# Kernel tuning notes

Hardware: AMD Instinct MI355X
Metric: run time of the kernel (lower is better)

## Reference

```python
import jax, jax.numpy as jnp
import numpy as np

N, E = 50000, 800000
D, H, EDIM, DFF = 128, 8, 16, 512
C = D // H  # per-head channels
NEG_SLOPE_GAT = 0.2
NEG_SLOPE = 0.01
EPS_LN = 1e-6


def layer_norm(x, g, b):
    mu = x.mean(-1, keepdims=True)
    sd = x.std(-1, keepdims=True, ddof=1)  # torch std default (unbiased)
    return g * (x - mu) / (sd + EPS_LN) + b


def gat_conv(x, ei, ew, W, a_src, a_dst, We, a_e, bias):
    # PyG GATConv with edge_dim, concat=True, eval mode (no dropout)
    n = x.shape[0]
    xh = (x @ W).reshape(n, H, C)            # [N,H,C]
    s_src = (xh * a_src).sum(-1)             # [N,H]
    s_dst = (xh * a_dst).sum(-1)             # [N,H]
    eh = (ew @ We).reshape(-1, H, C)         # [E,H,C]
    s_e = (eh * a_e).sum(-1)                 # [E,H]
    src, dst = ei[0], ei[1]
    alpha = jax.nn.leaky_relu(s_src[src] + s_dst[dst] + s_e, NEG_SLOPE_GAT)  # [E,H]
    # segment softmax over destination nodes
    m = jax.ops.segment_max(alpha, dst, num_segments=n)
    alpha = jnp.exp(alpha - m[dst])
    z = jax.ops.segment_sum(alpha, dst, num_segments=n)
    alpha = alpha / (z[dst] + 1e-16)
    msg = xh[src] * alpha[..., None]         # [E,H,C]
    out = jax.ops.segment_sum(msg, dst, num_segments=n)  # [N,H,C]
    return out.reshape(n, H * C) + bias


def setup_inputs() -> dict:
    key = jax.random.key(0)
    ks = jax.random.split(key, 32)
    p = lambda k, sh: (jax.random.normal(k, sh, dtype=jnp.float32) * 0.02)
    inp = {
        "nf": jax.random.normal(ks[0], (N, D), dtype=jnp.float32),
        "ei": jax.random.randint(ks[1], (2, E), 0, N, dtype=jnp.int32),
        "ew": jax.random.normal(ks[2], (E, EDIM), dtype=jnp.float32),
        # GATConv 1
        "W1": p(ks[3], (D, H * C)), "as1": p(ks[4], (H, C)), "ad1": p(ks[5], (H, C)),
        "We1": p(ks[6], (EDIM, H * C)), "ae1": p(ks[7], (H, C)), "b1": jnp.zeros((H * C,), jnp.float32),
        "g1": jnp.ones((D,), jnp.float32), "be1": jnp.zeros((D,), jnp.float32),
        # GATConv 2
        "W2": p(ks[8], (D, H * C)), "as2": p(ks[9], (H, C)), "ad2": p(ks[10], (H, C)),
        "We2": p(ks[11], (EDIM, H * C)), "ae2": p(ks[12], (H, C)), "b2": jnp.zeros((H * C,), jnp.float32),
        "g2": jnp.ones((D,), jnp.float32), "be2": jnp.zeros((D,), jnp.float32),
        # FFN + norm3
        "Wf1": p(ks[13], (D, DFF)), "bf1": jnp.zeros((DFF,), jnp.float32),
        "Wf2": p(ks[14], (DFF, D)), "bf2": jnp.zeros((D,), jnp.float32),
        "g3": jnp.ones((D,), jnp.float32), "be3": jnp.zeros((D,), jnp.float32),
    }
    return inp


def reference(nf, ei, ew, W1, as1, ad1, We1, ae1, b1, g1, be1,
              W2, as2, ad2, We2, ae2, b2, g2, be2,
              Wf1, bf1, Wf2, bf2, g3, be3):
    # gnn_mode == 'res', eval mode (dropout = identity)
    h = gat_conv(nf, ei, ew, W1, as1, ad1, We1, ae1, b1)
    nf = nf + jax.nn.leaky_relu(layer_norm(h, g1, be1), NEG_SLOPE)
    h = gat_conv(nf, ei, ew, W2, as2, ad2, We2, ae2, b2)
    nf = nf + jax.nn.leaky_relu(layer_norm(h, g2, be2), NEG_SLOPE)
    ff = jax.nn.relu(nf @ Wf1 + bf1) @ Wf2 + bf2
    nf = nf + jax.nn.leaky_relu(layer_norm(ff, g3, be3), NEG_SLOPE)
    return nf
```

## Files before the change

### kernel.cpp

```cpp
#include <hip/hip_runtime.h>
#include <hip/hip_bf16.h>

#define NN 50000
#define NE 800000
#define DD 128
#define HH 8
#define CC 16
#define DFF 512
#define ED 16
#define SCAN_NB ((NN + 255) / 256)

typedef __attribute__((ext_vector_type(8))) short bf16x8;
typedef __attribute__((ext_vector_type(4))) float f32x4;

union U8 { bf16x8 v; unsigned short s[8]; };

__device__ inline unsigned short f2bf(float f) {
    union { float f; unsigned u; } v; v.f = f;
    return (unsigned short)((v.u + 0x7fffu + ((v.u >> 16) & 1u)) >> 16);
}
__device__ inline float bf2f(unsigned s) {
    union { unsigned u; float f; } v; v.u = s << 16;
    return v.f;
}

__global__ void zero_int_k(int* __restrict__ a, int n) {
    int i = blockIdx.x * 256 + threadIdx.x;
    if (i < n) a[i] = 0;
}

__global__ void cvtpack_k(const float* __restrict__ W, unsigned short* __restrict__ Wpk,
                          int K, int N) {
    int idx = blockIdx.x * 256 + threadIdx.x;
    if (idx >= K * N) return;
    int e = idx & 7;
    int l = (idx >> 3) & 63;
    int r = idx >> 9;
    int n16 = N >> 4;
    int jc = r % n16;
    int kt = r / n16;
    int k = kt * 32 + (l >> 4) * 8 + e;
    int n = jc * 16 + (l & 15);
    Wpk[idx] = f2bf(W[(size_t)k * N + n]);
}

__global__ void count_k(const int* __restrict__ dst, int* __restrict__ cnt) {
    int e = blockIdx.x * 256 + threadIdx.x;
    if (e < NE) atomicAdd(&cnt[dst[e]], 1);
}

__global__ void blksum_k(const int* __restrict__ cnt, int* __restrict__ partials) {
    int i = blockIdx.x * 256 + threadIdx.x;
    int v = (i < NN) ? cnt[i] : 0;
#pragma unroll
    for (int m = 1; m < 64; m <<= 1) v += __shfl_xor(v, m, 64);
    __shared__ int ws[4];
    if ((threadIdx.x & 63) == 0) ws[threadIdx.x >> 6] = v;
    __syncthreads();
    if (threadIdx.x == 0) partials[blockIdx.x] = ws[0] + ws[1] + ws[2] + ws[3];
}

__global__ void scanpart_k(int* __restrict__ partials) {
    __shared__ int buf[256];
    int t = threadIdx.x;
    int v = (t < SCAN_NB) ? partials[t] : 0;
    buf[t] = v;
    __syncthreads();
    for (int off = 1; off < 256; off <<= 1) {
        int u = (t >= off) ? buf[t - off] : 0;
        __syncthreads();
        buf[t] += u;
        __syncthreads();
    }
    if (t < SCAN_NB) partials[t] = buf[t] - v;
}

__global__ void scanapply_k(const int* __restrict__ cnt, const int* __restrict__ partials,
                            int* __restrict__ row_start, int* __restrict__ cursor) {
    __shared__ int buf[256];
    int t = threadIdx.x;
    int i = blockIdx.x * 256 + t;
    int v = (i < NN) ? cnt[i] : 0;
    buf[t] = v;
    __syncthreads();
    for (int off = 1; off < 256; off <<= 1) {
        int u = (t >= off) ? buf[t - off] : 0;
        __syncthreads();
        buf[t] += u;
        __syncthreads();
    }
    int excl = buf[t] - v + partials[blockIdx.x];
    if (i < NN) {
        row_start[i] = excl;
        cursor[i] = excl;
        if (i == NN - 1) row_start[NN] = excl + v;
    }
}

__global__ void scatter_k(const int* __restrict__ ei, int* __restrict__ cursor,
                          int2* __restrict__ es_eid) {
    int e = blockIdx.x * 256 + threadIdx.x;
    if (e >= NE) return;
    int s = ei[e];
    int d = ei[NE + e];
    int pos = atomicAdd(&cursor[d], 1);
    es_eid[pos] = make_int2(s, e);
}

__global__ void se2_k(const float* __restrict__ ew, const int2* __restrict__ es_eid,
                      const float* __restrict__ We1, const float* __restrict__ ae1,
                      const float* __restrict__ We2, const float* __restrict__ ae2,
                      float* __restrict__ s_e1, float* __restrict__ s_e2) {
    __shared__ float A1[ED * HH], A2[ED * HH];
    int t = threadIdx.x;
    if (t < 128) {
        int k = t >> 3, h = t & 7;
        float s = 0.f;
#pragma unroll
        for (int c = 0; c < CC; c++) s += We1[k * DD + h * CC + c] * ae1[h * CC + c];
        A1[t] = s;
    } else {
        int u = t - 128;
        int k = u >> 3, h = u & 7;
        float s = 0.f;
#pragma unroll
        for (int c = 0; c < CC; c++) s += We2[k * DD + h * CC + c] * ae2[h * CC + c];
        A2[u] = s;
    }
    __syncthreads();
    int p = blockIdx.x * 256 + t;
    if (p >= NE) return;
    int eid = es_eid[p].y;
    const float* ep = &ew[(size_t)eid * ED];
    float4 v0 = *(const float4*)(ep);
    float4 v1 = *(const float4*)(ep + 4);
    float4 v2 = *(const float4*)(ep + 8);
    float4 v3 = *(const float4*)(ep + 12);
    float ev[16] = {v0.x, v0.y, v0.z, v0.w, v1.x, v1.y, v1.z, v1.w,
                    v2.x, v2.y, v2.z, v2.w, v3.x, v3.y, v3.z, v3.w};
    float o1[8] = {0, 0, 0, 0, 0, 0, 0, 0};
    float o2[8] = {0, 0, 0, 0, 0, 0, 0, 0};
#pragma unroll
    for (int k = 0; k < 16; k++) {
        float v = ev[k];
#pragma unroll
        for (int h = 0; h < 8; h++) {
            o1[h] += v * A1[k * 8 + h];
            o2[h] += v * A2[k * 8 + h];
        }
    }
    *(float4*)&s_e1[(size_t)p * 8]     = make_float4(o1[0], o1[1], o1[2], o1[3]);
    *(float4*)&s_e1[(size_t)p * 8 + 4] = make_float4(o1[4], o1[5], o1[6], o1[7]);
    *(float4*)&s_e2[(size_t)p * 8]     = make_float4(o2[0], o2[1], o2[2], o2[3]);
    *(float4*)&s_e2[(size_t)p * 8 + 4] = make_float4(o2[4], o2[5], o2[6], o2[7]);
}

__global__ __launch_bounds__(256) void gemm_mfma_k(const float* __restrict__ X,
                                                   const unsigned short* __restrict__ Wpk,
                                                   unsigned short* __restrict__ Ybf) {
    __shared__ char Xl[128 * 256];
    int t = threadIdx.x;
    int nb0 = blockIdx.x * 128;
    for (int c = t; c < 2048; c += 256) {
        int row = c >> 4, cb = c & 15;
        int n = nb0 + row;
        U8 u;
        if (n < NN) {
            const float* xp = &X[(size_t)n * DD + cb * 8];
            float4 a = *(const float4*)xp;
            float4 b = *(const float4*)(xp + 4);
            u.s[0] = f2bf(a.x); u.s[1] = f2bf(a.y); u.s[2] = f2bf(a.z); u.s[3] = f2bf(a.w);
            u.s[4] = f2bf(b.x); u.s[5] = f2bf(b.y); u.s[6] = f2bf(b.z); u.s[7] = f2bf(b.w);
        } else {
#pragma unroll
            for (int q = 0; q < 8; q++) u.s[q] = 0;
        }
        int byte = (row * 256 + cb * 16) ^ ((row & 7) << 4);
        *(bf16x8*)&Xl[byte] = u.v;
    }
    __syncthreads();
    int w = t >> 6, l = t & 63;
    int lrow = l & 15, lq = l >> 4;
    int r0 = (w & 1) * 64, c0 = (w >> 1) * 64;
    f32x4 acc[4][4];
#pragma unroll
    for (int i = 0; i < 4; i++)
#pragma unroll
        for (int j = 0; j < 4; j++) acc[i][j] = (f32x4){0.f, 0.f, 0.f, 0.f};
#pragma unroll
    for (int ks = 0; ks < 4; ks++) {
        int k0 = ks * 32;
        bf16x8 af[4], bq[4];
#pragma unroll
        for (int i = 0; i < 4; i++) {
            int rr = r0 + i * 16 + lrow;
            int byte = (rr * 256 + k0 * 2 + lq * 16) ^ ((rr & 7) << 4);
            af[i] = *(const bf16x8*)&Xl[byte];
        }
#pragma unroll
        for (int j = 0; j < 4; j++) {
            int j16 = (c0 >> 4) + j;
            bq[j] = *(const bf16x8*)&Wpk[(((size_t)ks * 8 + j16) * 64 + l) * 8];
        }
#pragma unroll
        for (int i = 0; i < 4; i++)
#pragma unroll
            for (int j = 0; j < 4; j++)
                acc[i][j] = __builtin_amdgcn_mfma_f32_16x16x32_bf16(af[i], bq[j], acc[i][j], 0, 0, 0);
    }
#pragma unroll
    for (int i = 0; i < 4; i++) {
#pragma unroll
        for (int j = 0; j < 4; j++) {
#pragma unroll
            for (int q = 0; q < 4; q++) {
                int n = nb0 + r0 + i * 16 + lq * 4 + q;
                if (n < NN) Ybf[(size_t)n * DD + c0 + j * 16 + lrow] = f2bf(acc[i][j][q]);
            }
        }
    }
}

__global__ void ssd_k(const unsigned short* __restrict__ xh_bf, const float* __restrict__ a_src,
                      const float* __restrict__ a_dst, float* __restrict__ s_src,
                      float* __restrict__ s_dst) {
    __shared__ float as[128], ad[128];
    if (threadIdx.x < 128) {
        as[threadIdx.x] = a_src[threadIdx.x];
        ad[threadIdx.x] = a_dst[threadIdx.x];
    }
    __syncthreads();
    int idx = blockIdx.x * 256 + threadIdx.x;
    if (idx >= NN * HH) return;
    int n = idx >> 3, h = idx & 7;
    const unsigned short* x = &xh_bf[(size_t)n * DD + h * CC];
    U8 u0, u1;
    u0.v = *(const bf16x8*)(x);
    u1.v = *(const bf16x8*)(x + 8);
    float s1 = 0.f, s2 = 0.f;
#pragma unroll
    for (int c = 0; c < 8; c++) {
        float v = bf2f(u0.s[c]);
        s1 += v * as[h * CC + c];
        s2 += v * ad[h * CC + c];
    }
#pragma unroll
    for (int c = 0; c < 8; c++) {
        float v = bf2f(u1.s[c]);
        s1 += v * as[h * CC + 8 + c];
        s2 += v * ad[h * CC + 8 + c];
    }
    s_src[idx] = s1;
    s_dst[idx] = s2;
}

__global__ __launch_bounds__(256) void agg_ln_k(const int* __restrict__ row_start,
                                                const int2* __restrict__ es_eid,
                                                const float* __restrict__ s_src,
                                                const float* __restrict__ s_dst,
                                                const float* __restrict__ s_e,
                                                const unsigned short* __restrict__ xh_bf,
                                                const float* __restrict__ bias,
                                                const float* __restrict__ g,
                                                const float* __restrict__ be,
                                                const float* __restrict__ res,
                                                float* __restrict__ outNf) {
    int wid = (blockIdx.x * 256 + threadIdx.x) >> 6;
    if (wid >= NN) return;
    int lane = threadIdx.x & 63;
    int h = lane >> 3;
    float sdst = s_dst[wid * 8 + h];
    int beg = row_start[wid], end = row_start[wid + 1];
    float acc0 = 0.f, acc1 = 0.f, z = 0.f;
    int p = beg;
    for (; p + 4 <= end; p += 4) {
        int q0 = es_eid[p].x;
        int q1 = es_eid[p + 1].x;
        int q2 = es_eid[p + 2].x;
        int q3 = es_eid[p + 3].x;
        float a0 = s_src[q0 * 8 + h] + sdst + s_e[(size_t)p * 8 + h];
        float a1 = s_src[q1 * 8 + h] + sdst + s_e[(size_t)(p + 1) * 8 + h];
        float a2 = s_src[q2 * 8 + h] + sdst + s_e[(size_t)(p + 2) * 8 + h];
        float a3 = s_src[q3 * 8 + h] + sdst + s_e[(size_t)(p + 3) * 8 + h];
        unsigned u0 = *(const unsigned*)&xh_bf[(size_t)q0 * DD + lane * 2];
        unsigned u1 = *(const unsigned*)&xh_bf[(size_t)q1 * DD + lane * 2];
        unsigned u2 = *(const unsigned*)&xh_bf[(size_t)q2 * DD + lane * 2];
        unsigned u3 = *(const unsigned*)&xh_bf[(size_t)q3 * DD + lane * 2];
        a0 = (a0 > 0.f) ? a0 : 0.2f * a0;
        a1 = (a1 > 0.f) ? a1 : 0.2f * a1;
        a2 = (a2 > 0.f) ? a2 : 0.2f * a2;
        a3 = (a3 > 0.f) ? a3 : 0.2f * a3;
        float e0 = __expf(a0);
        float e1 = __expf(a1);
        float e2 = __expf(a2);
        float e3 = __expf(a3);
        z += (e0 + e1) + (e2 + e3);
        acc0 = fmaf(e0, bf2f(u0 & 0xffffu), acc0);
        acc1 = fmaf(e0, bf2f(u0 >> 16), acc1);
        acc0 = fmaf(e1, bf2f(u1 & 0xffffu), acc0);
        acc1 = fmaf(e1, bf2f(u1 >> 16), acc1);
        acc0 = fmaf(e2, bf2f(u2 & 0xffffu), acc0);
        acc1 = fmaf(e2, bf2f(u2 >> 16), acc1);
        acc0 = fmaf(e3, bf2f(u3 & 0xffffu), acc0);
        acc1 = fmaf(e3, bf2f(u3 >> 16), acc1);
    }
    for (; p < end; p++) {
        int q0 = es_eid[p].x;
        float a0 = s_src[q0 * 8 + h] + sdst + s_e[(size_t)p * 8 + h];
        unsigned u0 = *(const unsigned*)&xh_bf[(size_t)q0 * DD + lane * 2];
        a0 = (a0 > 0.f) ? a0 : 0.2f * a0;
        float e0 = __expf(a0);
        z += e0;
        acc0 = fmaf(e0, bf2f(u0 & 0xffffu), acc0);
        acc1 = fmaf(e0, bf2f(u0 >> 16), acc1);
    }
    float inv = 1.f / (z + 1e-16f);
    float2 b = *(const float2*)&bias[lane * 2];
    float x0 = acc0 * inv + b.x;
    float x1 = acc1 * inv + b.y;
    float s = x0 + x1;
    float q = x0 * x0 + x1 * x1;
#pragma unroll
    for (int m = 1; m < 64; m <<= 1) {
        s += __shfl_xor(s, m, 64);
        q += __shfl_xor(q, m, 64);
    }
    float mu = s * (1.f / 128.f);
    float var = (q - 128.f * mu * mu) * (1.f / 127.f);
    float sd = sqrtf(fmaxf(var, 0.f));
    float invs = 1.f / (sd + 1e-6f);
    float2 gg = *(const float2*)&g[lane * 2];
    float2 bb = *(const float2*)&be[lane * 2];
    float y0 = gg.x * (x0 - mu) * invs + bb.x;
    float y1 = gg.y * (x1 - mu) * invs + bb.y;
    y0 = (y0 > 0.f) ? y0 : 0.01f * y0;
    y1 = (y1 > 0.f) ? y1 : 0.01f * y1;
    float2 r = *(const float2*)&res[(size_t)wid * DD + lane * 2];
    *(float2*)&outNf[(size_t)wid * DD + lane * 2] = make_float2(r.x + y0, r.y + y1);
}

__global__ __launch_bounds__(256) void ln_k(const float* __restrict__ hin,
                                            const float* __restrict__ bias,
                                            const float* __restrict__ g,
                                            const float* __restrict__ be,
                                            const float* __restrict__ res,
                                            float* __restrict__ out) {
    int wid = (blockIdx.x * 256 + threadIdx.x) >> 6;
    if (wid >= NN) return;
    int lane = threadIdx.x & 63;
    float2 x = *(const float2*)&hin[(size_t)wid * DD + lane * 2];
    float2 b = *(const float2*)&bias[lane * 2];
    x.x += b.x;
    x.y += b.y;
    float s = x.x + x.y;
    float q = x.x * x.x + x.y * x.y;
#pragma unroll
    for (int m = 1; m < 64; m <<= 1) {
        s += __shfl_xor(s, m, 64);
        q += __shfl_xor(q, m, 64);
    }
    float mu = s * (1.f / 128.f);
    float var = (q - 128.f * mu * mu) * (1.f / 127.f);
    float sd = sqrtf(fmaxf(var, 0.f));
    float inv = 1.f / (sd + 1e-6f);
    float2 gg = *(const float2*)&g[lane * 2];
    float2 bb = *(const float2*)&be[lane * 2];
    float y0 = gg.x * (x.x - mu) * inv + bb.x;
    float y1 = gg.y * (x.y - mu) * inv + bb.y;
    y0 = (y0 > 0.f) ? y0 : 0.01f * y0;
    y1 = (y1 > 0.f) ? y1 : 0.01f * y1;
    float2 r = *(const float2*)&res[(size_t)wid * DD + lane * 2];
    *(float2*)&out[(size_t)wid * DD + lane * 2] = make_float2(r.x + y0, r.y + y1);
}

__global__ __launch_bounds__(256) void ffn_mfma_k(const float* __restrict__ X,
                                                  const unsigned short* __restrict__ Wf1pk,
                                                  const float* __restrict__ bf1,
                                                  const unsigned short* __restrict__ Wf2pk,
                                                  float* __restrict__ out) {
    __shared__ char Xl[64 * 256];
    __shared__ char Hl[64 * 256];
    int t = threadIdx.x;
    int nb0 = blockIdx.x * 64;
    for (int c = t; c < 1024; c += 256) {
        int row = c >> 4, cb = c & 15;
        int n = nb0 + row;
        U8 u;
        if (n < NN) {
            const float* xp = &X[(size_t)n * DD + cb * 8];
            float4 a = *(const float4*)xp;
            float4 b = *(const float4*)(xp + 4);
            u.s[0] = f2bf(a.x); u.s[1] = f2bf(a.y); u.s[2] = f2bf(a.z); u.s[3] = f2bf(a.w);
            u.s[4] = f2bf(b.x); u.s[5] = f2bf(b.y); u.s[6] = f2bf(b.z); u.s[7] = f2bf(b.w);
        } else {
#pragma unroll
            for (int q = 0; q < 8; q++) u.s[q] = 0;
        }
        int byte = (row * 256 + cb * 16) ^ ((row & 7) << 4);
        *(bf16x8*)&Xl[byte] = u.v;
    }
    __syncthreads();
    int w = t >> 6, l = t & 63;
    int lrow = l & 15, lq = l >> 4;
    int wr = (w & 1) * 32;
    int wc = (w >> 1) * 64;
    f32x4 oacc[2][4];
#pragma unroll
    for (int i = 0; i < 2; i++)
#pragma unroll
        for (int j = 0; j < 4; j++) oacc[i][j] = (f32x4){0.f, 0.f, 0.f, 0.f};

#pragma unroll
    for (int ch = 0; ch < 4; ch++) {
        int hc0 = ch * 128;
        f32x4 a[2][4];
#pragma unroll
        for (int i = 0; i < 2; i++)
#pragma unroll
            for (int j = 0; j < 4; j++) a[i][j] = (f32x4){0.f, 0.f, 0.f, 0.f};
#pragma unroll
        for (int ks = 0; ks < 4; ks++) {
            int k0 = ks * 32;
            bf16x8 af[2], bq[4];
#pragma unroll
            for (int i = 0; i < 2; i++) {
                int rr = wr + i * 16 + lrow;
                int byte = (rr * 256 + k0 * 2 + lq * 16) ^ ((rr & 7) << 4);
                af[i] = *(const bf16x8*)&Xl[byte];
            }
#pragma unroll
            for (int j = 0; j < 4; j++) {
                int j16 = ch * 8 + (wc >> 4) + j;
                bq[j] = *(const bf16x8*)&Wf1pk[(((size_t)ks * 32 + j16) * 64 + l) * 8];
            }
#pragma unroll
            for (int i = 0; i < 2; i++)
#pragma unroll
                for (int j = 0; j < 4; j++)
                    a[i][j] = __builtin_amdgcn_mfma_f32_16x16x32_bf16(af[i], bq[j], a[i][j], 0, 0, 0);
        }
        float bias[4];
#pragma unroll
        for (int j = 0; j < 4; j++) bias[j] = bf1[hc0 + wc + j * 16 + lrow];
#pragma unroll
        for (int i = 0; i < 2; i++) {
#pragma unroll
            for (int j = 0; j < 4; j++) {
#pragma unroll
                for (int q = 0; q < 4; q++) {
                    float v = fmaxf(a[i][j][q] + bias[j], 0.f);
                    int row = wr + i * 16 + lq * 4 + q;
                    int col = wc + j * 16 + lrow;
                    int byte = (row * 256 + col * 2) ^ ((row & 7) << 4);
                    *(unsigned short*)&Hl[byte] = f2bf(v);
                }
            }
        }
        __syncthreads();
#pragma unroll
        for (int ks = 0; ks < 4; ks++) {
            int k0 = ks * 32;
            bf16x8 hf[2], b2[4];
#pragma unroll
            for (int i = 0; i < 2; i++) {
                int rr = wr + i * 16 + lrow;
                int byte = (rr * 256 + k0 * 2 + lq * 16) ^ ((rr & 7) << 4);
                hf[i] = *(const bf16x8*)&Hl[byte];
            }
#pragma unroll
            for (int j = 0; j < 4; j++) {
                int kt = ch * 4 + ks;
                int j16 = (wc >> 4) + j;
                b2[j] = *(const bf16x8*)&Wf2pk[(((size_t)kt * 8 + j16) * 64 + l) * 8];
            }
#pragma unroll
            for (int i = 0; i < 2; i++)
#pragma unroll
                for (int j = 0; j < 4; j++)
                    oacc[i][j] = __builtin_amdgcn_mfma_f32_16x16x32_bf16(hf[i], b2[j], oacc[i][j], 0, 0, 0);
        }
        __syncthreads();
    }
#pragma unroll
    for (int i = 0; i < 2; i++) {
#pragma unroll
        for (int j = 0; j < 4; j++) {
#pragma unroll
            for (int q = 0; q < 4; q++) {
                int n = nb0 + wr + i * 16 + lq * 4 + q;
                if (n < NN) out[(size_t)n * DD + wc + j * 16 + lrow] = oacc[i][j][q];
            }
        }
    }
}

extern "C" void kernel_launch(void* const* d_in, const int* in_sizes, int n_in,
                              void* d_out, int out_size, void* d_ws, size_t ws_size,
                              hipStream_t stream) {
    const float* nf  = (const float*)d_in[0];
    const int*   ei  = (const int*)d_in[1];
    const float* ew  = (const float*)d_in[2];
    const float* W1  = (const float*)d_in[3];
    const float* as1 = (const float*)d_in[4];
    const float* ad1 = (const float*)d_in[5];
    const float* We1 = (const float*)d_in[6];
    const float* ae1 = (const float*)d_in[7];
    const float* b1  = (const float*)d_in[8];
    const float* g1  = (const float*)d_in[9];
    const float* be1 = (const float*)d_in[10];
    const float* W2  = (const float*)d_in[11];
    const float* as2 = (const float*)d_in[12];
    const float* ad2 = (const float*)d_in[13];
    const float* We2 = (const float*)d_in[14];
    const float* ae2 = (const float*)d_in[15];
    const float* b2  = (const float*)d_in[16];
    const float* g2  = (const float*)d_in[17];
    const float* be2 = (const float*)d_in[18];
    const float* Wf1 = (const float*)d_in[19];
    const float* bf1 = (const float*)d_in[20];
    const float* Wf2 = (const float*)d_in[21];
    const float* bf2 = (const float*)d_in[22];
    const float* g3  = (const float*)d_in[23];
    const float* be3 = (const float*)d_in[24];
    float* out = (float*)d_out;

    char* p = (char*)d_ws;
    auto alloc = [&](size_t bytes) {
        char* r = p;
        p += (bytes + 255) & ~(size_t)255;
        return r;
    };
    float* nf_cur = (float*)alloc((size_t)NN * DD * 4);
    float* h_out  = (float*)alloc((size_t)NN * DD * 4);
    unsigned short* xh_bf = (unsigned short*)alloc((size_t)NN * DD * 2);
    float* s_e1   = (float*)alloc((size_t)NE * HH * 4);
    float* s_e2   = (float*)alloc((size_t)NE * HH * 4);
    float* s_src  = (float*)alloc((size_t)NN * HH * 4);
    float* s_dst  = (float*)alloc((size_t)NN * HH * 4);
    int* row_start = (int*)alloc((size_t)(NN + 1) * 4);
    int* cnt       = (int*)alloc((size_t)NN * 4);
    int* cursor    = (int*)alloc((size_t)NN * 4);
    int* partials  = (int*)alloc((size_t)SCAN_NB * 4);
    int2* es_eid   = (int2*)alloc((size_t)NE * 8);
    unsigned short* W1pk  = (unsigned short*)alloc((size_t)DD * DD * 2);
    unsigned short* W2pk  = (unsigned short*)alloc((size_t)DD * DD * 2);
    unsigned short* Wf1pk = (unsigned short*)alloc((size_t)DD * DFF * 2);
    unsigned short* Wf2pk = (unsigned short*)alloc((size_t)DFF * DD * 2);

    int ebl = (NE + 255) / 256;
    int nbl = (NN + 255) / 256;

    cvtpack_k<<<(DD * DD + 255) / 256, 256, 0, stream>>>(W1, W1pk, DD, DD);
    cvtpack_k<<<(DD * DD + 255) / 256, 256, 0, stream>>>(W2, W2pk, DD, DD);
    cvtpack_k<<<(DD * DFF + 255) / 256, 256, 0, stream>>>(Wf1, Wf1pk, DD, DFF);
    cvtpack_k<<<(DD * DFF + 255) / 256, 256, 0, stream>>>(Wf2, Wf2pk, DFF, DD);

    zero_int_k<<<nbl, 256, 0, stream>>>(cnt, NN);
    count_k<<<ebl, 256, 0, stream>>>(ei + NE, cnt);
    blksum_k<<<SCAN_NB, 256, 0, stream>>>(cnt, partials);
    scanpart_k<<<1, 256, 0, stream>>>(partials);
    scanapply_k<<<SCAN_NB, 256, 0, stream>>>(cnt, partials, row_start, cursor);
    scatter_k<<<ebl, 256, 0, stream>>>(ei, cursor, es_eid);

    se2_k<<<ebl, 256, 0, stream>>>(ew, es_eid, We1, ae1, We2, ae2, s_e1, s_e2);

    int gbl = (NN + 127) / 128;
    int wbl = (NN + 3) / 4;
    int sbl = (NN * HH + 255) / 256;

    gemm_mfma_k<<<gbl, 256, 0, stream>>>(nf, W1pk, xh_bf);
    ssd_k<<<sbl, 256, 0, stream>>>(xh_bf, as1, ad1, s_src, s_dst);
    agg_ln_k<<<wbl, 256, 0, stream>>>(row_start, es_eid, s_src, s_dst, s_e1, xh_bf,
                                      b1, g1, be1, nf, nf_cur);

    gemm_mfma_k<<<gbl, 256, 0, stream>>>(nf_cur, W2pk, xh_bf);
    ssd_k<<<sbl, 256, 0, stream>>>(xh_bf, as2, ad2, s_src, s_dst);
    agg_ln_k<<<wbl, 256, 0, stream>>>(row_start, es_eid, s_src, s_dst, s_e2, xh_bf,
                                      b2, g2, be2, nf_cur, nf_cur);

    ffn_mfma_k<<<(NN + 63) / 64, 256, 0, stream>>>(nf_cur, Wf1pk, bf1, Wf2pk, h_out);
    ln_k<<<wbl, 256, 0, stream>>>(h_out, bf2, g3, be3, nf_cur, out);
}
```

Before: 320.5 us.

## Replace global atomic CSR scatter with two-pass bucketed binning

```diff
diff --git a/kernel.cpp b/kernel.cpp
--- a/kernel.cpp
+++ b/kernel.cpp
@@ -9,6 +9,9 @@
 #define DFF 512
 #define ED 16
 #define SCAN_NB ((NN + 255) / 256)
+#define BKT 256
+#define NBKT ((NN + BKT - 1) / BKT)
+#define EPB 4096
 
 typedef __attribute__((ext_vector_type(8))) short bf16x8;
 typedef __attribute__((ext_vector_type(4))) float f32x4;
@@ -97,14 +100,55 @@
     }
 }
 
-__global__ void scatter_k(const int* __restrict__ ei, int* __restrict__ cursor,
-                          int2* __restrict__ es_eid) {
-    int e = blockIdx.x * 256 + threadIdx.x;
-    if (e >= NE) return;
-    int s = ei[e];
-    int d = ei[NE + e];
-    int pos = atomicAdd(&cursor[d], 1);
-    es_eid[pos] = make_int2(s, e);
+__global__ void bucketbase_k(const int* __restrict__ row_start, int* __restrict__ bucket_cursor) {
+    int b = blockIdx.x * 256 + threadIdx.x;
+    if (b < NBKT) bucket_cursor[b] = row_start[b * BKT];
+}
+
+__global__ __launch_bounds__(256) void bin_k(const int* __restrict__ ei,
+                                             int* __restrict__ bucket_cursor,
+                                             int2* __restrict__ binned) {
+    __shared__ int hist[NBKT];
+    __shared__ int base[NBKT];
+    int t = threadIdx.x;
+    int e0 = blockIdx.x * EPB;
+    int eend = e0 + EPB; if (eend > NE) eend = NE;
+    if (t < NBKT) hist[t] = 0;
+    __syncthreads();
+    for (int e = e0 + t; e < eend; e += 256) {
+        int d = ei[NE + e];
+        atomicAdd(&hist[d >> 8], 1);
+    }
+    __syncthreads();
+    if (t < NBKT) {
+        int c = hist[t];
+        base[t] = c ? atomicAdd(&bucket_cursor[t], c) : 0;
+        hist[t] = 0;
+    }
+    __syncthreads();
+    for (int e = e0 + t; e < eend; e += 256) {
+        int s = ei[e];
+        int d = ei[NE + e];
+        int b = d >> 8;
+        int loc = atomicAdd(&hist[b], 1);
+        binned[base[b] + loc] = make_int2(s | ((d & 255) << 16), e);
+    }
+}
+
+__global__ __launch_bounds__(256) void csr_scatter_k(const int2* __restrict__ binned,
+                                                     const int* __restrict__ row_start,
+                                                     int* __restrict__ cursor,
+                                                     int2* __restrict__ es_eid) {
+    int b = blockIdx.x;
+    int beg = row_start[b * BKT];
+    int endNode = (b + 1) * BKT; if (endNode > NN) endNode = NN;
+    int end = row_start[endNode];
+    for (int p = beg + threadIdx.x; p < end; p += 256) {
+        int2 r = binned[p];
+        int d = b * BKT + (r.x >> 16);
+        int pos = atomicAdd(&cursor[d], 1);
+        es_eid[pos] = make_int2(r.x & 0xffff, r.y);
+    }
 }
 
 __global__ void se2_k(const float* __restrict__ ew, const int2* __restrict__ es_eid,
@@ -531,7 +575,6 @@
         return r;
     };
     float* nf_cur = (float*)alloc((size_t)NN * DD * 4);
-    float* h_out  = (float*)alloc((size_t)NN * DD * 4);
     unsigned short* xh_bf = (unsigned short*)alloc((size_t)NN * DD * 2);
     float* s_e1   = (float*)alloc((size_t)NE * HH * 4);
     float* s_e2   = (float*)alloc((size_t)NE * HH * 4);
@@ -541,11 +584,14 @@
     int* cnt       = (int*)alloc((size_t)NN * 4);
     int* cursor    = (int*)alloc((size_t)NN * 4);
     int* partials  = (int*)alloc((size_t)SCAN_NB * 4);
+    int* bucket_cursor = (int*)alloc((size_t)NBKT * 4);
+    int2* binned   = (int2*)alloc((size_t)NE * 8);
     int2* es_eid   = (int2*)alloc((size_t)NE * 8);
     unsigned short* W1pk  = (unsigned short*)alloc((size_t)DD * DD * 2);
     unsigned short* W2pk  = (unsigned short*)alloc((size_t)DD * DD * 2);
     unsigned short* Wf1pk = (unsigned short*)alloc((size_t)DD * DFF * 2);
     unsigned short* Wf2pk = (unsigned short*)alloc((size_t)DFF * DD * 2);
+    float* h_out = s_e1;
 
     int ebl = (NE + 255) / 256;
     int nbl = (NN + 255) / 256;
@@ -560,7 +606,10 @@
     blksum_k<<<SCAN_NB, 256, 0, stream>>>(cnt, partials);
     scanpart_k<<<1, 256, 0, stream>>>(partials);
     scanapply_k<<<SCAN_NB, 256, 0, stream>>>(cnt, partials, row_start, cursor);
-    scatter_k<<<ebl, 256, 0, stream>>>(ei, cursor, es_eid);
+
+    bucketbase_k<<<(NBKT + 255) / 256, 256, 0, stream>>>(row_start, bucket_cursor);
+    bin_k<<<(NE + EPB - 1) / EPB, 256, 0, stream>>>(ei, bucket_cursor, binned);
+    csr_scatter_k<<<NBKT, 256, 0, stream>>>(binned, row_start, cursor, es_eid);
 
     se2_k<<<ebl, 256, 0, stream>>>(ew, es_eid, We1, ae1, We2, ae2, s_e1, s_e2);
 
```

Measured after the change: 303.3 us. 1.06x faster.
